# Optimization experiments

Hardware: AMD Instinct MI355X
Metric: run time of the kernel (lower is better)

## Reference

```python
import jax, jax.numpy as jnp
import numpy as np

B, CIN, HIN, WIN = 8192, 16, 6, 6
FM = 64                      # feature_maps
DK = FM // 2                 # 32
DV = FM // 2                 # 32
NH = FM // 2                 # 32 heads -> dkh = dvh = 1
OUT_CH = 5
HID = 128


def _conv2d(x, w, b, stride=1):
    # x: NCHW, w: OIHW, VALID padding (padding=(k-1)//2 = 0 for k=2)
    y = jax.lax.conv_general_dilated(
        x, w, window_strides=(stride, stride), padding='VALID',
        dimension_numbers=('NCHW', 'OIHW', 'NCHW'))
    return y + b[None, :, None, None]


def setup_inputs() -> dict:
    key = jax.random.key(0)
    ks = jax.random.split(key, 13)
    s = 0.1  # small init scale keeps softmax logits well-conditioned
    return {
        'x':      jax.random.normal(ks[0], (B, CIN, HIN, WIN), jnp.float32),
        # AugmentedConv: conv_out (out_channels - dv), qkv conv (2dk+dv), attn 1x1
        'conv_w': jax.random.normal(ks[1], (FM - DV, CIN, 2, 2), jnp.float32) * s,
        'conv_b': jax.random.normal(ks[2], (FM - DV,), jnp.float32) * s,
        'qkv_w':  jax.random.normal(ks[3], (2 * DK + DV, CIN, 2, 2), jnp.float32) * s,
        'qkv_b':  jax.random.normal(ks[4], (2 * DK + DV,), jnp.float32) * s,
        'attn_w': jax.random.normal(ks[5], (DV, DV, 1, 1), jnp.float32) * s,
        'attn_b': jax.random.normal(ks[6], (DV,), jnp.float32) * s,
        # DoubleDense: fm*5*5 -> hid -> hid//2 -> out
        'w1': jax.random.normal(ks[7], (HID, FM * 5 * 5), jnp.float32) * s,
        'b1': jax.random.normal(ks[8], (HID,), jnp.float32) * s,
        'w2': jax.random.normal(ks[9], (HID // 2, HID), jnp.float32) * s,
        'b2': jax.random.normal(ks[10], (HID // 2,), jnp.float32) * s,
        'w3': jax.random.normal(ks[11], (OUT_CH, HID // 2), jnp.float32) * s,
        'b3': jax.random.normal(ks[12], (OUT_CH,), jnp.float32) * s,
    }


def _forward(x, conv_w, conv_b, qkv_w, qkv_b, attn_w, attn_b, w1, b1, w2, b2, w3, b3):
    # ---- AugmentedConv ----
    conv_out = _conv2d(x, conv_w, conv_b)            # [B, FM-DV, 5, 5]
    qkv = _conv2d(x, qkv_w, qkv_b)                   # [B, 2DK+DV, 5, 5]
    b, _, h, w = qkv.shape
    q, k, v = jnp.split(qkv, [DK, 2 * DK], axis=1)
    dkh = DK // NH
    q = q * (dkh ** -0.5)
    flat_q = q.reshape(b, NH, dkh, h * w)            # [B, Nh, dkh, HW]
    flat_k = k.reshape(b, NH, dkh, h * w)
    flat_v = v.reshape(b, NH, DV // NH, h * w)
    # logits = q^T k over head-dim: [B, Nh, HW, HW]
    logits = jnp.einsum('bndi,bndj->bnij', flat_q, flat_k)
    weights = jax.nn.softmax(logits, axis=-1)
    # attn = weights @ v^T -> [B, Nh, HW, dvh]
    attn = jnp.einsum('bnij,bnjd->bnid', weights, flat_v.transpose(0, 1, 3, 2))
    # faithful to torch: raw reshape (B, Nh, dvh, H, W) then combine heads
    attn = attn.reshape(b, NH, DV // NH, h, w).reshape(b, DV, h, w)
    attn = _conv2d(attn, attn_w, attn_b)             # 1x1 conv
    y = jnp.concatenate([conv_out, attn], axis=1)    # [B, FM, 5, 5]
    # ---- ReLU + DoubleDense ----
    y = jax.nn.relu(y).reshape(b, -1)                # [B, FM*25]
    y = jax.nn.relu(y @ w1.T + b1)
    y = jax.nn.relu(y @ w2.T + b2)
    return y @ w3.T + b3                             # [B, OUT_CH]


def reference(x, conv_w, conv_b, qkv_w, qkv_b, attn_w, attn_b, w1, b1, w2, b2, w3, b3):
    return _forward(x, conv_w, conv_b, qkv_w, qkv_b, attn_w, attn_b,
                    w1, b1, w2, b2, w3, b3)
```

## Files before the change

### kernel.cpp

```cpp
#include <hip/hip_runtime.h>
#include <hip/hip_bf16.h>
#include <cstdint>
#include <cstddef>


typedef __attribute__((ext_vector_type(4))) float f32x4;
typedef __attribute__((ext_vector_type(2))) float f32x2;
typedef __attribute__((ext_vector_type(8))) __bf16 bf16x8;
typedef __attribute__((ext_vector_type(4))) __bf16 bf16x4;

#define LOG2E 1.4426950408889634f
#define ACT_STRIDE 1608
#define ACT_LDS_BYTES (32 * ACT_STRIDE * 2)
#define SCRATCH_OFF ACT_LDS_BYTES
#define LDS_TOTAL (ACT_LDS_BYTES + 8 * 7168)

__device__ __forceinline__ float fast_exp2(float x) {
#if __has_builtin(__builtin_amdgcn_exp2f)
  return __builtin_amdgcn_exp2f(x);
#else
  return __expf(x * 0.6931471805599453f);
#endif
}

__device__ __forceinline__ f32x4 mfma16(bf16x8 a, bf16x8 b, f32x4 c) {
  return __builtin_amdgcn_mfma_f32_16x16x32_bf16(a, b, c, 0, 0, 0);
}

__global__ __launch_bounds__(64) void prep(
    const float* __restrict__ conv_w, const float* __restrict__ conv_b,
    const float* __restrict__ qkv_w,  const float* __restrict__ qkv_b,
    const float* __restrict__ attn_w,
    const float* __restrict__ w1, const float* __restrict__ w2,
    __hip_bfloat16* __restrict__ wqb, float* __restrict__ biasb,
    __hip_bfloat16* __restrict__ wab,
    __hip_bfloat16* __restrict__ w1bp, __hip_bfloat16* __restrict__ w2b) {
  const int t = threadIdx.x, tb = blockIdx.x;
  if (tb < 16) {
#pragma unroll
    for (int j = 0; j < 8; ++j) {
      int i = tb * 512 + j * 64 + t;
      float w = (i < 2048) ? conv_w[i] : qkv_w[i - 2048];
      if (i >= 4096 && i < 6144) w *= LOG2E;
      wqb[i] = __float2bfloat16(w);
    }
  } else if (tb == 16) {
#pragma unroll
    for (int j = 0; j < 16; ++j) wab[j * 64 + t] = __float2bfloat16(attn_w[j * 64 + t]);
    for (int i = t; i < 128; i += 64) {
      float b = (i < 32) ? conv_b[i] : qkv_b[i - 32];
      if (i >= 64 && i < 96) b *= LOG2E;
      biasb[i] = b;
    }
  } else if (tb < 145) {
    const int u = tb - 17;
    __shared__ float rowf[1600];
    const float* wr = w1 + u * 1600;
#pragma unroll
    for (int j = 0; j < 25; ++j) rowf[j * 64 + t] = wr[j * 64 + t];
    __hip_bfloat16* wo = w1bp + u * 1600;
#pragma unroll
    for (int j = 0; j < 25; ++j) {
      wo[j * 64 + t] = __float2bfloat16(rowf[t * 25 + j]);
    }
  } else {
#pragma unroll
    for (int j = 0; j < 64; ++j) {
      int i = (tb - 145) * 4096 + j * 64 + t;
      w2b[i] = __float2bfloat16(w2[i]);
    }
  }
}

__global__ __launch_bounds__(512) void kf(
    const float* __restrict__ x,
    const float* __restrict__ biasb,
    const __hip_bfloat16* __restrict__ wqb,
    const __hip_bfloat16* __restrict__ wab, const float* __restrict__ attn_b,
    const __hip_bfloat16* __restrict__ w1bp, const float* __restrict__ b1,
    const __hip_bfloat16* __restrict__ w2b, const float* __restrict__ b2,
    const float* __restrict__ w3, const float* __restrict__ b3,
    float* __restrict__ out) {
  extern __shared__ __align__(16) char lds_all[];
  const int t = threadIdx.x & 63;
  const int wv = threadIdx.x >> 6;
  const int l15 = t & 15, quad = t >> 4;

  __hip_bfloat16* act_lds = (__hip_bfloat16*)lds_all;
  char* my = lds_all + SCRATCH_OFF + wv * 7168;
  __bf16* xs  = (__bf16*)my;
  __bf16* as_ = (__bf16*)my;
  __bf16* qs  = (__bf16*)(my + 1600);

  bf16x8 bfr[8][2];
#pragma unroll
  for (int nt = 0; nt < 8; ++nt)
#pragma unroll
    for (int ks = 0; ks < 2; ++ks)
      bfr[nt][ks] = *(const bf16x8*)((const __bf16*)wqb + (nt * 16 + l15) * 64 + ks * 32 + quad * 8);
  float bias[8];
#pragma unroll
  for (int nt = 0; nt < 8; ++nt) bias[nt] = biasb[nt * 16 + l15];
  bf16x8 bw[2]; float ab[2];
#pragma unroll
  for (int nt2 = 0; nt2 < 2; ++nt2) {
    int n = nt2 * 16 + l15;
    bw[nt2] = *(const bf16x8*)((const __bf16*)wab + n * 32 + quad * 8);
    ab[nt2] = attn_b[n];
  }

  const int b_base = blockIdx.x * 32 + wv * 4;

  float xr[9];
  {
    const float* xb = x + (size_t)b_base * 576;
#pragma unroll
    for (int i = 0; i < 9; ++i) xr[i] = xb[t + i * 64];
  }

  for (int it = 0; it < 4; ++it) {
    const int rowoff = (wv * 4 + it) * ACT_STRIDE;

#pragma unroll
    for (int i = 0; i < 9; ++i) xs[t + i * 64] = __float2bfloat16(xr[i]);

#pragma unroll
    for (int mt = 0; mt < 2; ++mt) {
      int row = mt * 16 + l15;
      int pos = row < 24 ? row : 24;
      int ii = pos / 5, jj = pos - ii * 5;
      const __bf16* xp = xs + ii * 6 + jj;
      bf16x8 af[2];
#pragma unroll
      for (int ks = 0; ks < 2; ++ks) {
        const __bf16* p0 = xp + (ks * 8 + quad * 2) * 36;
        bf16x8 a;
        a[0] = p0[0];  a[1] = p0[1];  a[2] = p0[6];  a[3] = p0[7];
        a[4] = p0[36]; a[5] = p0[37]; a[6] = p0[42]; a[7] = p0[43];
        af[ks] = a;
      }
      f32x4 acc[8];
#pragma unroll
      for (int nt = 0; nt < 8; ++nt) acc[nt] = (f32x4){0.f, 0.f, 0.f, 0.f};
#pragma unroll
      for (int ks = 0; ks < 2; ++ks)
#pragma unroll
        for (int nt = 0; nt < 8; ++nt)
          acc[nt] = mfma16(af[ks], bfr[nt][ks], acc[nt]);

#pragma unroll
      for (int r = 0; r < 4; ++r) {
        int orow = mt * 16 + quad * 4 + r;
        if (orow < 25) {
#pragma unroll
          for (int nt = 0; nt < 8; ++nt) {
            float v = acc[nt][r] + bias[nt];
            if (nt < 2) {
              act_lds[rowoff + orow * 64 + nt * 16 + l15] =
                  __float2bfloat16(fmaxf(v, 0.f));
            } else {
              qs[((nt - 2) * 16 + l15) * 28 + orow] = __float2bfloat16(v);
            }
          }
        }
      }
    }

    if (it < 3) {
      const float* xb = x + (size_t)(b_base + it + 1) * 576;
#pragma unroll
      for (int i = 0; i < 9; ++i) xr[i] = xb[t + i * 64];
    }

    {
      const int n = t & 31, half = t >> 5;
      const __bf16* qp = qs + n * 28;
      const __bf16* kp = qs + (32 + n) * 28;
      const __bf16* vp = qs + (64 + n) * 28;
      f32x2 kl2[12], vv2[12];
      float kl24, vv24;
#pragma unroll
      for (int c4 = 0; c4 < 6; ++c4) {
        bf16x4 bb = *(const bf16x4*)(kp + c4 * 4);
        bf16x4 cc = *(const bf16x4*)(vp + c4 * 4);
        kl2[c4 * 2]     = (f32x2){(float)bb[0], (float)bb[1]};
        kl2[c4 * 2 + 1] = (f32x2){(float)bb[2], (float)bb[3]};
        vv2[c4 * 2]     = (f32x2){(float)cc[0], (float)cc[1]};
        vv2[c4 * 2 + 1] = (f32x2){(float)cc[2], (float)cc[3]};
      }
      kl24 = (float)kp[24]; vv24 = (float)vp[24];

      const int i0 = half * 12;
      float qv[13];
      {
        const __bf16* qbase = qp + i0;
        bf16x4 q0 = *(const bf16x4*)(qbase);
        bf16x4 q1 = *(const bf16x4*)(qbase + 4);
        bf16x4 q2 = *(const bf16x4*)(qbase + 8);
#pragma unroll
        for (int z = 0; z < 4; ++z) {
          qv[z] = (float)q0[z]; qv[4 + z] = (float)q1[z]; qv[8 + z] = (float)q2[z];
        }
        qv[12] = (float)qbase[12];
      }

#pragma unroll
      for (int z = 0; z < 13; ++z) {
        const float qi = qv[z];
        const f32x2 qi2 = {qi, qi};
        f32x2 sA = {0.f, 0.f}, sB = {0.f, 0.f};
        f32x2 oA = {0.f, 0.f}, oB = {0.f, 0.f};
        float s4 = 0.f, o4 = 0.f;
#pragma unroll
        for (int p = 0; p < 6; ++p) {
          f32x2 mA = qi2 * kl2[p];
          f32x2 mB = qi2 * kl2[p + 6];
          f32x2 eA = {fast_exp2(mA.x), fast_exp2(mA.y)};
          f32x2 eB = {fast_exp2(mB.x), fast_exp2(mB.y)};
          sA += eA;
          sB += eB;
          oA = eA * vv2[p] + oA;
          oB = eB * vv2[p + 6] + oB;
        }
        {
          float e = fast_exp2(qi * kl24);
          s4 += e;
          o4 = __builtin_fmaf(e, vv24, o4);
        }
        float ss = ((sA.x + sA.y) + (sB.x + sB.y)) + s4;
        float oo = ((oA.x + oA.y) + (oB.x + oB.y)) + o4;
        as_[(i0 + z) * 32 + n] = __float2bfloat16(oo * __builtin_amdgcn_rcpf(ss));
      }
    }

    {
#pragma unroll
      for (int mt = 0; mt < 2; ++mt) {
        int row = mt * 16 + l15;
        int rc = row < 24 ? row : 24;
        bf16x8 af = *(const bf16x8*)(as_ + rc * 32 + quad * 8);
        f32x4 acc[2];
#pragma unroll
        for (int nt2 = 0; nt2 < 2; ++nt2)
          acc[nt2] = mfma16(af, bw[nt2], (f32x4){0.f, 0.f, 0.f, 0.f});
#pragma unroll
        for (int r = 0; r < 4; ++r) {
          int orow = mt * 16 + quad * 4 + r;
          if (orow < 25) {
#pragma unroll
            for (int nt2 = 0; nt2 < 2; ++nt2)
              act_lds[rowoff + orow * 64 + 32 + nt2 * 16 + l15] =
                  __float2bfloat16(fmaxf(acc[nt2][r] + ab[nt2], 0.f));
          }
        }
      }
    }
  }

  __syncthreads();

  const int wave = threadIdx.x >> 6;
  const int wm = wave >> 2;
  const int wn = wave & 3;
  const int b0 = blockIdx.x * 32;

  __hip_bfloat16* C1s = (__hip_bfloat16*)(lds_all + SCRATCH_OFF);
  __hip_bfloat16* C2s = (__hip_bfloat16*)(lds_all + SCRATCH_OFF + 8704);

  f32x4 acc0 = {0.f, 0.f, 0.f, 0.f};
  f32x4 acc1 = {0.f, 0.f, 0.f, 0.f};
  {
    const __bf16* aL    = (const __bf16*)act_lds + (wm * 16 + l15) * ACT_STRIDE + quad * 8;
    const __bf16* bptr0 = (const __bf16*)w1bp + (size_t)(wn * 32 + l15) * 1600 + quad * 8;
    const __bf16* bptr1 = bptr0 + 16 * 1600;
#pragma unroll 5
    for (int k0 = 0; k0 < 1600; k0 += 32) {
      bf16x8 av  = *(const bf16x8*)(aL + k0);
      bf16x8 bv0 = *(const bf16x8*)(bptr0 + k0);
      bf16x8 bv1 = *(const bf16x8*)(bptr1 + k0);
      acc0 = mfma16(av, bv0, acc0);
      acc1 = mfma16(av, bv1, acc1);
    }
  }
  {
    const int col0 = wn * 32 + l15;
    const float bias0 = b1[col0];
    const float bias1 = b1[col0 + 16];
#pragma unroll
    for (int r = 0; r < 4; ++r) {
      const int row = wm * 16 + quad * 4 + r;
      C1s[row * 136 + col0]      = __float2bfloat16(fmaxf(acc0[r] + bias0, 0.f));
      C1s[row * 136 + col0 + 16] = __float2bfloat16(fmaxf(acc1[r] + bias1, 0.f));
    }
  }
  __syncthreads();

  f32x4 acc2 = {0.f, 0.f, 0.f, 0.f};
  {
    const __bf16* aL = (const __bf16*)C1s + (wm * 16 + l15) * 136 + quad * 8;
    const __bf16* bL = (const __bf16*)w2b + (wn * 16 + l15) * 128 + quad * 8;
#pragma unroll
    for (int k0 = 0; k0 < 128; k0 += 32)
      acc2 = mfma16(*(const bf16x8*)(aL + k0), *(const bf16x8*)(bL + k0), acc2);
  }
  {
    const int col = wn * 16 + l15;
    const float bias = b2[col];
#pragma unroll
    for (int r = 0; r < 4; ++r) {
      const int row = wm * 16 + quad * 4 + r;
      C2s[row * 72 + col] = __float2bfloat16(fmaxf(acc2[r] + bias, 0.f));
    }
  }
  __syncthreads();

  if (threadIdx.x < 160) {
    const int row = threadIdx.x / 5;
    const int oc = threadIdx.x - row * 5;
    float s = b3[oc];
#pragma unroll
    for (int k = 0; k < 64; ++k)
      s += __bfloat162float(C2s[row * 72 + k]) * w3[oc * 64 + k];
    out[(size_t)(b0 + row) * 5 + oc] = s;
  }
}

extern "C" void kernel_launch(void* const* d_in, const int* in_sizes, int n_in,
                              void* d_out, int out_size, void* d_ws, size_t ws_size,
                              hipStream_t stream) {
  const float* x      = (const float*)d_in[0];
  const float* conv_w = (const float*)d_in[1];
  const float* conv_b = (const float*)d_in[2];
  const float* qkv_w  = (const float*)d_in[3];
  const float* qkv_b  = (const float*)d_in[4];
  const float* attn_w = (const float*)d_in[5];
  const float* attn_b = (const float*)d_in[6];
  const float* w1 = (const float*)d_in[7];
  const float* b1 = (const float*)d_in[8];
  const float* w2 = (const float*)d_in[9];
  const float* b2 = (const float*)d_in[10];
  const float* w3 = (const float*)d_in[11];
  const float* b3 = (const float*)d_in[12];
  float* out = (float*)d_out;

  char* ws = (char*)d_ws;
  __hip_bfloat16* w1bp  = (__hip_bfloat16*)ws;
  __hip_bfloat16* w2b   = (__hip_bfloat16*)(ws + 409600);
  __hip_bfloat16* wqb   = (__hip_bfloat16*)(ws + 425984);
  float*          biasb = (float*)(ws + 442368);
  __hip_bfloat16* wab   = (__hip_bfloat16*)(ws + 442880);

  hipFuncSetAttribute(reinterpret_cast<const void*>(kf),
                      hipFuncAttributeMaxDynamicSharedMemorySize, LDS_TOTAL);

  prep<<<dim3(147), dim3(64), 0, stream>>>(conv_w, conv_b, qkv_w, qkv_b, attn_w,
                                           w1, w2, wqb, biasb, wab, w1bp, w2b);
  kf<<<dim3(256), dim3(512), LDS_TOTAL, stream>>>(x, biasb, wqb, wab, attn_b,
                                                  w1bp, b1, w2b, b2, w3, b3, out);
}
```

Baseline: 148.3 us.

## Software-pipeline per-wave conv, attention and projection stages across samples

Restructures the per-wave four-sample loop into a software pipeline. The next sample's x is loaded and gathered and its QKV MFMA is issued while the current sample's attention softmax and projection finish, with global loads prefetched two samples ahead. Attention output is written in place into the q slot, so the per-wave scratch shrinks and the projection gathers its A fragment with strided scalar LDS reads. The goal is to hide global and LDS latency and overlap MFMA with VALU exp work, at the cost of higher register pressure and a less efficient gather in the projection step.

```diff
diff --git a/kernel.cpp b/kernel.cpp
--- a/kernel.cpp
+++ b/kernel.cpp
@@ -12,8 +12,8 @@
 #define LOG2E 1.4426950408889634f
 #define ACT_STRIDE 1608
 #define ACT_LDS_BYTES (32 * ACT_STRIDE * 2)
-#define SCRATCH_OFF ACT_LDS_BYTES
-#define LDS_TOTAL (ACT_LDS_BYTES + 8 * 7168)
+#define SCRATCH_PER_WAVE 6528
+#define LDS_TOTAL (ACT_LDS_BYTES + 8 * SCRATCH_PER_WAVE)
 
 __device__ __forceinline__ float fast_exp2(float x) {
 #if __has_builtin(__builtin_amdgcn_exp2f)
@@ -25,6 +25,150 @@
 
 __device__ __forceinline__ f32x4 mfma16(bf16x8 a, bf16x8 b, f32x4 c) {
   return __builtin_amdgcn_mfma_f32_16x16x32_bf16(a, b, c, 0, 0, 0);
+}
+
+
+__device__ __forceinline__ void stage_x(__bf16* xs, const float xr[9], int t) {
+#pragma unroll
+  for (int i = 0; i < 9; ++i) xs[t + i * 64] = __float2bfloat16(xr[i]);
+}
+
+__device__ __forceinline__ void gather_af(const __bf16* xs, int l15, int quad,
+                                          bf16x8 afg[2][2]) {
+#pragma unroll
+  for (int mt = 0; mt < 2; ++mt) {
+    int row = mt * 16 + l15;
+    int pos = row < 24 ? row : 24;
+    int ii = pos / 5, jj = pos - ii * 5;
+    const __bf16* xp = xs + ii * 6 + jj;
+#pragma unroll
+    for (int ks = 0; ks < 2; ++ks) {
+      const __bf16* p0 = xp + (ks * 8 + quad * 2) * 36;
+      bf16x8 a;
+      a[0] = p0[0];  a[1] = p0[1];  a[2] = p0[6];  a[3] = p0[7];
+      a[4] = p0[36]; a[5] = p0[37]; a[6] = p0[42]; a[7] = p0[43];
+      afg[mt][ks] = a;
+    }
+  }
+}
+
+__device__ __forceinline__ void mfma_epi(const bf16x8 afg[2][2], const bf16x8 bfr[8][2],
+                                         const float bias[8], __bf16* qs,
+                                         __hip_bfloat16* act_lds, int rowoff,
+                                         int l15, int quad) {
+#pragma unroll
+  for (int mt = 0; mt < 2; ++mt) {
+    f32x4 acc[8];
+#pragma unroll
+    for (int nt = 0; nt < 8; ++nt) acc[nt] = (f32x4){0.f, 0.f, 0.f, 0.f};
+#pragma unroll
+    for (int ks = 0; ks < 2; ++ks)
+#pragma unroll
+      for (int nt = 0; nt < 8; ++nt)
+        acc[nt] = mfma16(afg[mt][ks], bfr[nt][ks], acc[nt]);
+#pragma unroll
+    for (int r = 0; r < 4; ++r) {
+      int orow = mt * 16 + quad * 4 + r;
+      if (orow < 25) {
+#pragma unroll
+        for (int nt = 0; nt < 8; ++nt) {
+          float v = acc[nt][r] + bias[nt];
+          if (nt < 2) {
+            act_lds[rowoff + orow * 64 + nt * 16 + l15] =
+                __float2bfloat16(fmaxf(v, 0.f));
+          } else {
+            qs[((nt - 2) * 16 + l15) * 28 + orow] = __float2bfloat16(v);
+          }
+        }
+      }
+    }
+  }
+}
+
+__device__ __forceinline__ void attn_load(const __bf16* qs, int n, int i0,
+                                          f32x2 kl2[12], f32x2 vv2[12],
+                                          float& kl24, float& vv24, float qv[13]) {
+  const __bf16* qp = qs + n * 28;
+  const __bf16* kp = qs + (32 + n) * 28;
+  const __bf16* vp = qs + (64 + n) * 28;
+#pragma unroll
+  for (int c4 = 0; c4 < 6; ++c4) {
+    bf16x4 bb = *(const bf16x4*)(kp + c4 * 4);
+    bf16x4 cc = *(const bf16x4*)(vp + c4 * 4);
+    kl2[c4 * 2]     = (f32x2){(float)bb[0], (float)bb[1]};
+    kl2[c4 * 2 + 1] = (f32x2){(float)bb[2], (float)bb[3]};
+    vv2[c4 * 2]     = (f32x2){(float)cc[0], (float)cc[1]};
+    vv2[c4 * 2 + 1] = (f32x2){(float)cc[2], (float)cc[3]};
+  }
+  kl24 = (float)kp[24]; vv24 = (float)vp[24];
+  const __bf16* qbase = qp + i0;
+  bf16x4 q0 = *(const bf16x4*)(qbase);
+  bf16x4 q1 = *(const bf16x4*)(qbase + 4);
+  bf16x4 q2 = *(const bf16x4*)(qbase + 8);
+#pragma unroll
+  for (int z = 0; z < 4; ++z) {
+    qv[z] = (float)q0[z]; qv[4 + z] = (float)q1[z]; qv[8 + z] = (float)q2[z];
+  }
+  qv[12] = (float)qbase[12];
+}
+
+__device__ __forceinline__ void attn_compute(__bf16* qs, const f32x2 kl2[12],
+                                             const f32x2 vv2[12], float kl24, float vv24,
+                                             const float qv[13], int n, int i0) {
+#pragma unroll
+  for (int z = 0; z < 13; ++z) {
+    const float qi = qv[z];
+    const f32x2 qi2 = {qi, qi};
+    f32x2 sA = {0.f, 0.f}, sB = {0.f, 0.f};
+    f32x2 oA = {0.f, 0.f}, oB = {0.f, 0.f};
+    float s4 = 0.f, o4 = 0.f;
+#pragma unroll
+    for (int p = 0; p < 6; ++p) {
+      f32x2 mA = qi2 * kl2[p];
+      f32x2 mB = qi2 * kl2[p + 6];
+      f32x2 eA = {fast_exp2(mA.x), fast_exp2(mA.y)};
+      f32x2 eB = {fast_exp2(mB.x), fast_exp2(mB.y)};
+      sA += eA;
+      sB += eB;
+      oA = eA * vv2[p] + oA;
+      oB = eB * vv2[p + 6] + oB;
+    }
+    {
+      float e = fast_exp2(qi * kl24);
+      s4 += e;
+      o4 = __builtin_fmaf(e, vv24, o4);
+    }
+    float ss = ((sA.x + sA.y) + (sB.x + sB.y)) + s4;
+    float oo = ((oA.x + oA.y) + (oB.x + oB.y)) + o4;
+    qs[n * 28 + i0 + z] = __float2bfloat16(oo * __builtin_amdgcn_rcpf(ss));
+  }
+}
+
+__device__ __forceinline__ void phase3(const __bf16* qs, const bf16x8 bw[2],
+                                       const float ab[2], __hip_bfloat16* act_lds,
+                                       int rowoff, int l15, int quad) {
+#pragma unroll
+  for (int mt = 0; mt < 2; ++mt) {
+    int row = mt * 16 + l15;
+    int rc = row < 24 ? row : 24;
+    bf16x8 af;
+#pragma unroll
+    for (int j = 0; j < 8; ++j) af[j] = qs[(quad * 8 + j) * 28 + rc];
+    f32x4 acc[2];
+#pragma unroll
+    for (int nt2 = 0; nt2 < 2; ++nt2)
+      acc[nt2] = mfma16(af, bw[nt2], (f32x4){0.f, 0.f, 0.f, 0.f});
+#pragma unroll
+    for (int r = 0; r < 4; ++r) {
+      int orow = mt * 16 + quad * 4 + r;
+      if (orow < 25) {
+#pragma unroll
+        for (int nt2 = 0; nt2 < 2; ++nt2)
+          act_lds[rowoff + orow * 64 + 32 + nt2 * 16 + l15] =
+              __float2bfloat16(fmaxf(acc[nt2][r] + ab[nt2], 0.f));
+      }
+    }
+  }
 }
 
 __global__ __launch_bounds__(64) void prep(
@@ -87,10 +231,9 @@
   const int l15 = t & 15, quad = t >> 4;
 
   __hip_bfloat16* act_lds = (__hip_bfloat16*)lds_all;
-  char* my = lds_all + SCRATCH_OFF + wv * 7168;
-  __bf16* xs  = (__bf16*)my;
-  __bf16* as_ = (__bf16*)my;
-  __bf16* qs  = (__bf16*)(my + 1600);
+  char* my = lds_all + ACT_LDS_BYTES + wv * SCRATCH_PER_WAVE;
+  __bf16* xs = (__bf16*)my;
+  __bf16* qs = (__bf16*)(my + 1152);
 
   bf16x8 bfr[8][2];
 #pragma unroll
@@ -104,156 +247,53 @@
   bf16x8 bw[2]; float ab[2];
 #pragma unroll
   for (int nt2 = 0; nt2 < 2; ++nt2) {
-    int n = nt2 * 16 + l15;
-    bw[nt2] = *(const bf16x8*)((const __bf16*)wab + n * 32 + quad * 8);
-    ab[nt2] = attn_b[n];
+    int nn = nt2 * 16 + l15;
+    bw[nt2] = *(const bf16x8*)((const __bf16*)wab + nn * 32 + quad * 8);
+    ab[nt2] = attn_b[nn];
   }
 
   const int b_base = blockIdx.x * 32 + wv * 4;
-
-  float xr[9];
+  const int n = t & 31, half = t >> 5;
+  const int i0 = half * 12;
+
+  float xrA[9];
+  bf16x8 afg[2][2];
+  f32x2 kl2[12], vv2[12];
+  float kl24, vv24, qv[13];
+
   {
     const float* xb = x + (size_t)b_base * 576;
 #pragma unroll
-    for (int i = 0; i < 9; ++i) xr[i] = xb[t + i * 64];
-  }
-
+    for (int i = 0; i < 9; ++i) xrA[i] = xb[t + i * 64];
+  }
+  stage_x(xs, xrA, t);
+  gather_af(xs, l15, quad, afg);
+  {
+    const float* xb = x + (size_t)(b_base + 1) * 576;
+#pragma unroll
+    for (int i = 0; i < 9; ++i) xrA[i] = xb[t + i * 64];
+  }
+  mfma_epi(afg, bfr, bias, qs, act_lds, (wv * 4 + 0) * ACT_STRIDE, l15, quad);
+  stage_x(xs, xrA, t);
+  gather_af(xs, l15, quad, afg);
+  attn_load(qs, n, i0, kl2, vv2, kl24, vv24, qv);
+
+#pragma unroll 1
   for (int it = 0; it < 4; ++it) {
-    const int rowoff = (wv * 4 + it) * ACT_STRIDE;
-
-#pragma unroll
-    for (int i = 0; i < 9; ++i) xs[t + i * 64] = __float2bfloat16(xr[i]);
-
-#pragma unroll
-    for (int mt = 0; mt < 2; ++mt) {
-      int row = mt * 16 + l15;
-      int pos = row < 24 ? row : 24;
-      int ii = pos / 5, jj = pos - ii * 5;
-      const __bf16* xp = xs + ii * 6 + jj;
-      bf16x8 af[2];
-#pragma unroll
-      for (int ks = 0; ks < 2; ++ks) {
-        const __bf16* p0 = xp + (ks * 8 + quad * 2) * 36;
-        bf16x8 a;
-        a[0] = p0[0];  a[1] = p0[1];  a[2] = p0[6];  a[3] = p0[7];
-        a[4] = p0[36]; a[5] = p0[37]; a[6] = p0[42]; a[7] = p0[43];
-        af[ks] = a;
+    if (it < 2) {
+      const float* xb = x + (size_t)(b_base + it + 2) * 576;
+#pragma unroll
+      for (int i = 0; i < 9; ++i) xrA[i] = xb[t + i * 64];
+    }
+    attn_compute(qs, kl2, vv2, kl24, vv24, qv, n, i0);
+    phase3(qs, bw, ab, act_lds, (wv * 4 + it) * ACT_STRIDE, l15, quad);
+    if (it < 3) {
+      mfma_epi(afg, bfr, bias, qs, act_lds, (wv * 4 + it + 1) * ACT_STRIDE, l15, quad);
+      if (it < 2) {
+        stage_x(xs, xrA, t);
+        gather_af(xs, l15, quad, afg);
       }
-      f32x4 acc[8];
-#pragma unroll
-      for (int nt = 0; nt < 8; ++nt) acc[nt] = (f32x4){0.f, 0.f, 0.f, 0.f};
-#pragma unroll
-      for (int ks = 0; ks < 2; ++ks)
-#pragma unroll
-        for (int nt = 0; nt < 8; ++nt)
-          acc[nt] = mfma16(af[ks], bfr[nt][ks], acc[nt]);
-
-#pragma unroll
-      for (int r = 0; r < 4; ++r) {
-        int orow = mt * 16 + quad * 4 + r;
-        if (orow < 25) {
-#pragma unroll
-          for (int nt = 0; nt < 8; ++nt) {
-            float v = acc[nt][r] + bias[nt];
-            if (nt < 2) {
-              act_lds[rowoff + orow * 64 + nt * 16 + l15] =
-                  __float2bfloat16(fmaxf(v, 0.f));
-            } else {
-              qs[((nt - 2) * 16 + l15) * 28 + orow] = __float2bfloat16(v);
-            }
-          }
-        }
-      }
-    }
-
-    if (it < 3) {
-      const float* xb = x + (size_t)(b_base + it + 1) * 576;
-#pragma unroll
-      for (int i = 0; i < 9; ++i) xr[i] = xb[t + i * 64];
-    }
-
-    {
-      const int n = t & 31, half = t >> 5;
-      const __bf16* qp = qs + n * 28;
-      const __bf16* kp = qs + (32 + n) * 28;
-      const __bf16* vp = qs + (64 + n) * 28;
-      f32x2 kl2[12], vv2[12];
-      float kl24, vv24;
-#pragma unroll
-      for (int c4 = 0; c4 < 6; ++c4) {
-        bf16x4 bb = *(const bf16x4*)(kp + c4 * 4);
-        bf16x4 cc = *(const bf16x4*)(vp + c4 * 4);
-        kl2[c4 * 2]     = (f32x2){(float)bb[0], (float)bb[1]};
-        kl2[c4 * 2 + 1] = (f32x2){(float)bb[2], (float)bb[3]};
-        vv2[c4 * 2]     = (f32x2){(float)cc[0], (float)cc[1]};
-        vv2[c4 * 2 + 1] = (f32x2){(float)cc[2], (float)cc[3]};
-      }
-      kl24 = (float)kp[24]; vv24 = (float)vp[24];
-
-      const int i0 = half * 12;
-      float qv[13];
-      {
-        const __bf16* qbase = qp + i0;
-        bf16x4 q0 = *(const bf16x4*)(qbase);
-        bf16x4 q1 = *(const bf16x4*)(qbase + 4);
-        bf16x4 q2 = *(const bf16x4*)(qbase + 8);
-#pragma unroll
-        for (int z = 0; z < 4; ++z) {
-          qv[z] = (float)q0[z]; qv[4 + z] = (float)q1[z]; qv[8 + z] = (float)q2[z];
-        }
-        qv[12] = (float)qbase[12];
-      }
-
-#pragma unroll
-      for (int z = 0; z < 13; ++z) {
-        const float qi = qv[z];
-        const f32x2 qi2 = {qi, qi};
-        f32x2 sA = {0.f, 0.f}, sB = {0.f, 0.f};
-        f32x2 oA = {0.f, 0.f}, oB = {0.f, 0.f};
-        float s4 = 0.f, o4 = 0.f;
-#pragma unroll
-        for (int p = 0; p < 6; ++p) {
-          f32x2 mA = qi2 * kl2[p];
-          f32x2 mB = qi2 * kl2[p + 6];
-          f32x2 eA = {fast_exp2(mA.x), fast_exp2(mA.y)};
-          f32x2 eB = {fast_exp2(mB.x), fast_exp2(mB.y)};
-          sA += eA;
-          sB += eB;
-          oA = eA * vv2[p] + oA;
-          oB = eB * vv2[p + 6] + oB;
-        }
-        {
-          float e = fast_exp2(qi * kl24);
-          s4 += e;
-          o4 = __builtin_fmaf(e, vv24, o4);
-        }
-        float ss = ((sA.x + sA.y) + (sB.x + sB.y)) + s4;
-        float oo = ((oA.x + oA.y) + (oB.x + oB.y)) + o4;
-        as_[(i0 + z) * 32 + n] = __float2bfloat16(oo * __builtin_amdgcn_rcpf(ss));
-      }
-    }
-
-    {
-#pragma unroll
-      for (int mt = 0; mt < 2; ++mt) {
-        int row = mt * 16 + l15;
-        int rc = row < 24 ? row : 24;
-        bf16x8 af = *(const bf16x8*)(as_ + rc * 32 + quad * 8);
-        f32x4 acc[2];
-#pragma unroll
-        for (int nt2 = 0; nt2 < 2; ++nt2)
-          acc[nt2] = mfma16(af, bw[nt2], (f32x4){0.f, 0.f, 0.f, 0.f});
-#pragma unroll
-        for (int r = 0; r < 4; ++r) {
-          int orow = mt * 16 + quad * 4 + r;
-          if (orow < 25) {
-#pragma unroll
-            for (int nt2 = 0; nt2 < 2; ++nt2)
-              act_lds[rowoff + orow * 64 + 32 + nt2 * 16 + l15] =
-                  __float2bfloat16(fmaxf(acc[nt2][r] + ab[nt2], 0.f));
-          }
-        }
-      }
+      attn_load(qs, n, i0, kl2, vv2, kl24, vv24, qv);
     }
   }
 
@@ -264,8 +304,8 @@
   const int wn = wave & 3;
   const int b0 = blockIdx.x * 32;
 
-  __hip_bfloat16* C1s = (__hip_bfloat16*)(lds_all + SCRATCH_OFF);
-  __hip_bfloat16* C2s = (__hip_bfloat16*)(lds_all + SCRATCH_OFF + 8704);
+  __hip_bfloat16* C1s = (__hip_bfloat16*)(lds_all + ACT_LDS_BYTES);
+  __hip_bfloat16* C2s = (__hip_bfloat16*)(lds_all + ACT_LDS_BYTES + 8704);
 
   f32x4 acc0 = {0.f, 0.f, 0.f, 0.f};
   f32x4 acc1 = {0.f, 0.f, 0.f, 0.f};
```

After: 148.9 us. Within noise of the previous version (+0.4%).
